# Kernel tuning notes

Measured on AMD Instinct MI355X. Metric: run time of the kernel, lower is better.

The kernel has to match this reference:

```python
import jax, jax.numpy as jnp
import numpy as np

N, DIN, D, K, H, N_ITERS = 16384, 256, 1024, 64, 2048, 3
THRESH = 0.3
EPS = 1e-8


def layernorm(x):
    mu = jnp.mean(x, axis=-1, keepdims=True)
    var = jnp.var(x, axis=-1, keepdims=True)
    return (x - mu) * jax.lax.rsqrt(var + 1e-5)


def setup_inputs() -> dict:
    key = jax.random.key(0)
    ks = jax.random.split(key, 20)
    s = 0.02
    return {
        "detections_t": jax.random.normal(ks[0], (N, DIN), jnp.float32),
        "detections_t1": jax.random.normal(ks[1], (N, DIN), jnp.float32),
        "W_enc": s * jax.random.normal(ks[2], (DIN, D), jnp.float32),
        "b_enc": jnp.zeros((D,), jnp.float32),
        "Wq": s * jax.random.normal(ks[3], (D, D), jnp.float32),
        "bq": jnp.zeros((D,), jnp.float32),
        "Wk": s * jax.random.normal(ks[4], (D, D), jnp.float32),
        "bk": jnp.zeros((D,), jnp.float32),
        "Wv": s * jax.random.normal(ks[5], (D, D), jnp.float32),
        "bv": jnp.zeros((D,), jnp.float32),
        "Wi": s * jax.random.normal(ks[6], (3 * D, D), jnp.float32),  # GRU input weights
        "Wh": s * jax.random.normal(ks[7], (3 * D, D), jnp.float32),  # GRU hidden weights
        "bi": jnp.zeros((3 * D,), jnp.float32),
        "bh": jnp.zeros((3 * D,), jnp.float32),
        "W1": s * jax.random.normal(ks[8], (D, H), jnp.float32),
        "b1": jnp.zeros((H,), jnp.float32),
        "W2": s * jax.random.normal(ks[9], (H, D), jnp.float32),
        "b2": jnp.zeros((D,), jnp.float32),
        "slots_mu": s * jax.random.normal(ks[10], (1, D), jnp.float32),
        "init_noise": jax.random.normal(ks[11], (K, D), jnp.float32) * s,
    }


def _gru(u, h, Wi, Wh, bi, bh):
    gi = u @ Wi.T + bi          # [K, 3D]
    gh = h @ Wh.T + bh
    ir, iz, inn = jnp.split(gi, 3, axis=-1)
    hr, hz, hn = jnp.split(gh, 3, axis=-1)
    r = jax.nn.sigmoid(ir + hr)
    z = jax.nn.sigmoid(iz + hz)
    n = jnp.tanh(inn + r * hn)
    return (1.0 - z) * n + z * h


def _process_frame(dets, prev_slots, p):
    x = layernorm(dets @ p["W_enc"] + p["b_enc"])          # [N, D]
    k = x @ p["Wk"] + p["bk"]                               # [N, D]
    v = x @ p["Wv"] + p["bv"]                               # [N, D]
    slots = prev_slots if prev_slots is not None else p["slots_mu"] + p["init_noise"]
    scale = D ** -0.5
    for _ in range(N_ITERS):
        slots_prev = slots
        q = layernorm(slots) @ p["Wq"] + p["bq"]            # [K, D]
        dots = (q @ k.T) * scale                             # [K, N]
        attn = jax.nn.softmax(dots, axis=0)                  # slots compete per detection
        attn = attn / (jnp.sum(attn, axis=-1, keepdims=True) + EPS)
        updates = attn @ v                                   # [K, D]
        slots = _gru(updates, slots_prev, p["Wi"], p["Wh"], p["bi"], p["bh"])
        slots = slots + (jax.nn.relu(layernorm(slots) @ p["W1"] + p["b1"]) @ p["W2"] + p["b2"])
    return slots


def _slot_similarity(a, b):
    an = a / (jnp.linalg.norm(a, axis=-1, keepdims=True) + EPS)
    bn = b / (jnp.linalg.norm(b, axis=-1, keepdims=True) + EPS)
    return an @ bn.T                                         # [K, K]


def _greedy_match(sim):
    max_sims = jnp.max(sim, axis=1)
    max_idxs = jnp.argmax(sim, axis=1)
    order = jnp.argsort(-max_sims)
    def step(carry, idx):
        matches, used = carry
        j = max_idxs[idx]
        ok = jnp.logical_and(~used[j], max_sims[idx] > THRESH)
        matches = matches.at[idx].set(jnp.where(ok, j, matches[idx]))
        used = used.at[j].set(used[j] | ok)
        return (matches, used), None
    init = (jnp.full((K,), -1, jnp.int32), jnp.zeros((K,), jnp.bool_))
    (matches, _), _ = jax.lax.scan(step, init, order)
    return matches


def reference(detections_t, detections_t1, W_enc, b_enc, Wq, bq, Wk, bk, Wv, bv,
              Wi, Wh, bi, bh, W1, b1, W2, b2, slots_mu, init_noise):
    p = dict(W_enc=W_enc, b_enc=b_enc, Wq=Wq, bq=bq, Wk=Wk, bk=bk, Wv=Wv, bv=bv,
             Wi=Wi, Wh=Wh, bi=bi, bh=bh, W1=W1, b1=b1, W2=W2, b2=b2,
             slots_mu=slots_mu, init_noise=init_noise)
    prev_slots = _process_frame(detections_t, None, p)
    curr_slots = _process_frame(detections_t1, prev_slots, p)
    sim = _slot_similarity(prev_slots, curr_slots)
    matches = _greedy_match(sim)
    return matches, sim
```

## Files before the change

kernel.cpp:

```cpp
#include <hip/hip_runtime.h>
#include <hip/hip_bf16.h>
#include <type_traits>

typedef __hip_bfloat16 bf16;
typedef __attribute__((ext_vector_type(8))) short s16x8;
typedef __attribute__((ext_vector_type(4))) float f32x4;

#define N_DET 16384
#define DIN   256
#define DD    1024
#define KSLOT 64
#define HH    2048
#define TD    3072

__device__ __forceinline__ float b2f(bf16 x){ return __bfloat162float(x); }
__device__ __forceinline__ bf16  f2b(float x){ return __float2bfloat16(x); }
__device__ __forceinline__ float bits2f(short u){ return __uint_as_float(((unsigned)(unsigned short)u) << 16); }

__device__ __forceinline__ void gload_lds16(const void* g, void* l) {
  __builtin_amdgcn_global_load_lds(
      (const __attribute__((address_space(1))) unsigned int*)g,
      (__attribute__((address_space(3))) unsigned int*)l, 16, 0, 0);
}

__device__ __forceinline__ void big_compute(bf16* As, bf16* Bs,
    const bf16* __restrict__ Ap, const bf16* __restrict__ Bp, int K, f32x4 acc[4][4])
{
  const int tid = threadIdx.x;
  const int lane = tid & 63, wave = tid >> 6;
  const int wr = wave >> 1, wc = wave & 1;
  const int l15 = lane & 15, h = lane >> 4;
  const int rr = tid >> 3;
  const int qs = ((tid & 7) ^ (rr & 7)) * 8;

#pragma unroll
  for (int m = 0; m < 4; ++m)
#pragma unroll
    for (int n = 0; n < 4; ++n) acc[m][n] = {0.f, 0.f, 0.f, 0.f};

  for (int k0 = 0; k0 < K; k0 += 64) {
    __syncthreads();
#pragma unroll
    for (int g = 0; g < 4; ++g)
      gload_lds16(Ap + (size_t)(g * 32 + rr) * K + k0 + qs,
                  As + ((size_t)g * 256 + wave * 64) * 8);
#pragma unroll
    for (int g = 0; g < 4; ++g)
      gload_lds16(Bp + (size_t)(g * 32 + rr) * K + k0 + qs,
                  Bs + ((size_t)g * 256 + wave * 64) * 8);
    __syncthreads();

#pragma unroll
    for (int ks = 0; ks < 2; ++ks) {
      s16x8 af[4], bfr[4];
#pragma unroll
      for (int m = 0; m < 4; ++m) {
        int row = wr * 64 + m * 16 + l15;
        af[m] = *(const s16x8*)&As[row * 64 + (((ks * 4 + h) ^ (l15 & 7)) * 8)];
      }
#pragma unroll
      for (int n = 0; n < 4; ++n) {
        int row = wc * 64 + n * 16 + l15;
        bfr[n] = *(const s16x8*)&Bs[row * 64 + (((ks * 4 + h) ^ (l15 & 7)) * 8)];
      }
#pragma unroll
      for (int m = 0; m < 4; ++m)
#pragma unroll
        for (int n = 0; n < 4; ++n)
          acc[m][n] = __builtin_amdgcn_mfma_f32_16x16x32_bf16(af[m], bfr[n], acc[m][n], 0, 0, 0);
    }
  }
}

__device__ __forceinline__ void big_gemm_body(int wg, int nct,
    const bf16* __restrict__ A, const bf16* __restrict__ Bt,
    const float* __restrict__ bias, bf16* __restrict__ C, int N, int K,
    bf16* As, bf16* Bs)
{
  const int bn = (wg % nct) * 128;
  const int bm = (wg / nct) * 128;
  f32x4 acc[4][4];
  big_compute(As, Bs, A + (size_t)bm * K, Bt + (size_t)bn * K, K, acc);

  const int lane = threadIdx.x & 63, wave = threadIdx.x >> 6;
  const int wr = wave >> 1, wc = wave & 1;
#pragma unroll
  for (int m = 0; m < 4; ++m)
#pragma unroll
    for (int n = 0; n < 4; ++n) {
      int col = bn + wc * 64 + n * 16 + (lane & 15);
      float bv = bias ? bias[col] : 0.f;
#pragma unroll
      for (int j = 0; j < 4; ++j) {
        int row = bm + wr * 64 + m * 16 + (lane >> 4) * 4 + j;
        C[(size_t)row * N + col] = f2b(acc[m][n][j] + bv);
      }
    }
}

__global__ __launch_bounds__(256) void gemm_mfma_bt(
    const bf16* __restrict__ A, const bf16* __restrict__ Bt,
    const float* __restrict__ bias, bf16* __restrict__ C, int M, int N, int K)
{
  const int nct = N >> 7;
  const int chunk = gridDim.x >> 3;
  const int wg = (blockIdx.x & 7) * chunk + (blockIdx.x >> 3);
  __shared__ bf16 As[128 * 64];
  __shared__ bf16 Bs[128 * 64];
  big_gemm_body(wg, nct, A, Bt, bias, C, N, K, As, Bs);
}

__global__ __launch_bounds__(256) void gemm_setup_pair(
    const bf16* __restrict__ Wi_b, const bf16* __restrict__ Wv_bf, bf16* __restrict__ Wvit,
    const bf16* __restrict__ Wk_bf, const bf16* __restrict__ Wq_bf, bf16* __restrict__ Wqk_t)
{
  __shared__ bf16 As[128 * 64];
  __shared__ bf16 Bs[128 * 64];
  if (blockIdx.x < 192) {
    int bid = blockIdx.x;
    int wg = (bid & 7) * 24 + (bid >> 3);
    big_gemm_body(wg, 8, Wi_b, Wv_bf, nullptr, Wvit, DD, DD, As, Bs);
  } else {
    int bid = blockIdx.x - 192;
    int wg = (bid & 7) * 8 + (bid >> 3);
    big_gemm_body(wg, 8, Wk_bf, Wq_bf, nullptr, Wqk_t, DD, DD, As, Bs);
  }
}

__device__ __forceinline__ void skinny_compute(bf16* As, bf16* Bs,
    const bf16* __restrict__ A, const bf16* __restrict__ Bt,
    int K, int Kc, int n0, int kb0, f32x4 acc[4])
{
  const int tid = threadIdx.x;
  const int lane = tid & 63, wave = tid >> 6;
  const int rem = wave * 64 + lane;
  const int r = rem >> 2, q = rem & 3;
  const int l15 = lane & 15, h = lane >> 4;

#pragma unroll
  for (int m = 0; m < 4; ++m) acc[m] = {0.f, 0.f, 0.f, 0.f};

  for (int kb = kb0; kb < kb0 + Kc; kb += 128) {
    __syncthreads();
#pragma unroll
    for (int g = 0; g < 4; ++g)
      gload_lds16(A + (size_t)r * K + kb + g * 32 + q * 8,
                  As + ((size_t)g * 256 + wave * 64) * 8);
#pragma unroll
    for (int g = 0; g < 4; ++g)
      gload_lds16(Bt + (size_t)(n0 + r) * K + kb + g * 32 + q * 8,
                  Bs + ((size_t)g * 256 + wave * 64) * 8);
    __syncthreads();

#pragma unroll
    for (int ks = 0; ks < 4; ++ks) {
      s16x8 bfr = *(const s16x8*)&Bs[(ks * 64 + wave * 16 + l15) * 32 + h * 8];
#pragma unroll
      for (int m = 0; m < 4; ++m) {
        s16x8 af = *(const s16x8*)&As[(ks * 64 + m * 16 + l15) * 32 + h * 8];
        acc[m] = __builtin_amdgcn_mfma_f32_16x16x32_bf16(af, bfr, acc[m], 0, 0, 0);
      }
    }
  }
}

template<int EPI>
__global__ __launch_bounds__(256) void gemm_skinny_e(
    const bf16* __restrict__ A, const bf16* __restrict__ Bt,
    float* __restrict__ pbuf, bf16* __restrict__ outb,
    const float* __restrict__ bias, int N, int K, int Kc)
{
  __shared__ bf16 As[4 * 64 * 32];
  __shared__ bf16 Bs[4 * 64 * 32];
  f32x4 acc[4];
  skinny_compute(As, Bs, A, Bt, K, Kc, blockIdx.x * 64, blockIdx.y * Kc, acc);

  const int lane = threadIdx.x & 63, wave = threadIdx.x >> 6;
  const int l15 = lane & 15, h = lane >> 4;
#pragma unroll
  for (int m = 0; m < 4; ++m)
#pragma unroll
    for (int j = 0; j < 4; ++j) {
      int row = m * 16 + h * 4 + j;
      int col = blockIdx.x * 64 + wave * 16 + l15;
      if (EPI == 0) {
        pbuf[((size_t)(blockIdx.y * 64) + row) * N + col] = acc[m][j];
      } else {
        float v = acc[m][j] + bias[col];
        if (EPI == 2) v = fmaxf(v, 0.f);
        outb[(size_t)row * N + col] = f2b(v);
      }
    }
}

__global__ __launch_bounds__(256) void gemm_skinny_dual(
    const bf16* __restrict__ A0, const bf16* __restrict__ A1,
    const bf16* __restrict__ B0, const bf16* __restrict__ B1,
    float* __restrict__ p0, float* __restrict__ p1, int N, int K, int Kc)
{
  __shared__ bf16 As[4 * 64 * 32];
  __shared__ bf16 Bs[4 * 64 * 32];
  const bf16* A = blockIdx.z ? A1 : A0;
  const bf16* B = blockIdx.z ? B1 : B0;
  float* p = blockIdx.z ? p1 : p0;

  f32x4 acc[4];
  skinny_compute(As, Bs, A, B, K, Kc, blockIdx.x * 64, blockIdx.y * Kc, acc);

  const int lane = threadIdx.x & 63, wave = threadIdx.x >> 6;
  const int l15 = lane & 15, h = lane >> 4;
#pragma unroll
  for (int m = 0; m < 4; ++m)
#pragma unroll
    for (int j = 0; j < 4; ++j) {
      int row = m * 16 + h * 4 + j;
      int col = blockIdx.x * 64 + wave * 16 + l15;
      p[((size_t)(blockIdx.y * 64) + row) * N + col] = acc[m][j];
    }
}

__device__ __forceinline__ void block_ln_store(float v[4], float s, float sq,
    bf16* __restrict__ out, int row,
    const float* __restrict__ wqbk, float* __restrict__ cbuf, float* __restrict__ colsum)
{
  for (int o = 32; o > 0; o >>= 1) { s += __shfl_down(s, o, 64); sq += __shfl_down(sq, o, 64); }
  __shared__ float ls[4], lq[4];
  int w = threadIdx.x >> 6;
  if ((threadIdx.x & 63) == 0) { ls[w] = s; lq[w] = sq; }
  __syncthreads();
  s  = ls[0] + ls[1] + ls[2] + ls[3];
  sq = lq[0] + lq[1] + lq[2] + lq[3];
  float mu = s * (1.f / DD);
  float var = sq * (1.f / DD) - mu * mu;
  float rstd = rsqrtf(var + 1e-5f);
#pragma unroll
  for (int j = 0; j < 4; j++)
    out[(size_t)row * DD + threadIdx.x + j * 256] = f2b((v[j] - mu) * rstd);
  if (wqbk) {
    float dot = 0.f;
#pragma unroll
    for (int j = 0; j < 4; j++) dot += (v[j] - mu) * rstd * wqbk[threadIdx.x + j * 256];
    for (int o = 32; o > 0; o >>= 1) dot += __shfl_down(dot, o, 64);
    __syncthreads();
    if ((threadIdx.x & 63) == 0) ls[w] = dot;
    __syncthreads();
    if (threadIdx.x == 0) { cbuf[row] = ls[0] + ls[1] + ls[2] + ls[3]; colsum[row] = 0.f; }
  }
}

__global__ __launch_bounds__(256) void gru_reduce_ln(const float* __restrict__ pA,
    const float* __restrict__ pB, const float* __restrict__ bvi,
    const float* __restrict__ bh, float* __restrict__ slots, bf16* __restrict__ lnb)
{
  int s = blockIdx.x, t = threadIdx.x;
  float v[4], sum = 0.f, sq = 0.f;
#pragma unroll
  for (int j = 0; j < 4; ++j) {
    int d = t + j * 256;
    const float* a = pA + (size_t)s * TD;
    const float* b = pB + (size_t)s * TD;
    float ir = bvi[d] + a[d], iz = bvi[1024 + d] + a[1024 + d], in_ = bvi[2048 + d] + a[2048 + d];
    float hr = bh[d] + b[d], hz = bh[1024 + d] + b[1024 + d], hnn = bh[2048 + d] + b[2048 + d];
    float r = 1.f / (1.f + expf(-(ir + hr)));
    float z = 1.f / (1.f + expf(-(iz + hz)));
    float nn = tanhf(in_ + r * hnn);
    float h = slots[(size_t)s * DD + d];
    float hv = (1.f - z) * nn + z * h;
    slots[(size_t)s * DD + d] = hv;
    v[j] = hv; sum += hv; sq += hv * hv;
  }
  block_ln_store(v, sum, sq, lnb, s, nullptr, nullptr, nullptr);
}

template<int SK>
__global__ __launch_bounds__(256) void mlp2_reduce_ln(const float* __restrict__ pbuf,
    const float* __restrict__ bias, float* __restrict__ slots,
    bf16* __restrict__ slotspb, bf16* __restrict__ lnb,
    const float* __restrict__ wqbk, float* __restrict__ cbuf, float* __restrict__ colsum)
{
  int s = blockIdx.x, t = threadIdx.x;
  float v[4], sum = 0.f, sq = 0.f;
#pragma unroll
  for (int j = 0; j < 4; ++j) {
    int d = t + j * 256;
    float x = bias[d] + slots[(size_t)s * DD + d];
#pragma unroll
    for (int sk = 0; sk < SK; ++sk) x += pbuf[(size_t)(sk * 64 + s) * DD + d];
    slots[(size_t)s * DD + d] = x;
    slotspb[(size_t)s * DD + d] = f2b(x);
    v[j] = x; sum += x; sq += x * x;
  }
  block_ln_store(v, sum, sq, lnb, s, wqbk, cbuf, colsum);
}

__global__ __launch_bounds__(256) void slots_init_ln(const float* __restrict__ mu,
    const float* __restrict__ noise, float* __restrict__ slots,
    bf16* __restrict__ slotspb, bf16* __restrict__ lnb,
    const float* __restrict__ wqbk, float* __restrict__ cbuf, float* __restrict__ colsum)
{
  int s = blockIdx.x, t = threadIdx.x;
  float v[4], sum = 0.f, sq = 0.f;
#pragma unroll
  for (int j = 0; j < 4; ++j) {
    int d = t + j * 256;
    float x = mu[d] + noise[(size_t)s * DD + d];
    slots[(size_t)s * DD + d] = x;
    slotspb[(size_t)s * DD + d] = f2b(x);
    v[j] = x; sum += x; sq += x * x;
  }
  block_ln_store(v, sum, sq, lnb, s, wqbk, cbuf, colsum);
}

__global__ __launch_bounds__(256) void qk_softmax(const bf16* __restrict__ qkb,
    const bf16* __restrict__ x, const float* __restrict__ cbuf,
    bf16* __restrict__ attn, float* __restrict__ colsum)
{
  __shared__ bf16 Qs[64 * 64];
  __shared__ bf16 Ks[64 * 64];
  __shared__ float cs[64], cl[64];
  const int t = threadIdx.x, lane = t & 63, wave = t >> 6;
  const int n0 = blockIdx.x * 64;
  const int l15 = lane & 15, h = lane >> 4;
  if (t < 64) { cs[t] = 0.f; cl[t] = cbuf[t]; }

  f32x4 acc[4];
#pragma unroll
  for (int m = 0; m < 4; ++m) acc[m] = {0.f, 0.f, 0.f, 0.f};

  for (int k0 = 0; k0 < DD; k0 += 64) {
    __syncthreads();
#pragma unroll
    for (int c = 0; c < 2; ++c) {
      int i = c * 256 + t;
      int r = i >> 3, q8 = i & 7;
      gload_lds16(qkb + (size_t)r * DD + k0 + q8 * 8, Qs + ((size_t)c * 256 + wave * 64) * 8);
    }
#pragma unroll
    for (int c = 0; c < 2; ++c) {
      int i = c * 256 + t;
      int r = i >> 3, q8 = i & 7;
      gload_lds16(x + (size_t)(n0 + r) * DD + k0 + q8 * 8, Ks + ((size_t)c * 256 + wave * 64) * 8);
    }
    __syncthreads();

#pragma unroll
    for (int ks = 0; ks < 2; ++ks) {
      s16x8 bfr = *(const s16x8*)&Ks[(wave * 16 + l15) * 64 + ks * 32 + h * 8];
#pragma unroll
      for (int m = 0; m < 4; ++m) {
        s16x8 af = *(const s16x8*)&Qs[(m * 16 + l15) * 64 + ks * 32 + h * 8];
        acc[m] = __builtin_amdgcn_mfma_f32_16x16x32_bf16(af, bfr, acc[m], 0, 0, 0);
      }
    }
  }

  float e[4][4];
  float cmax = -1e30f;
#pragma unroll
  for (int m = 0; m < 4; ++m)
#pragma unroll
    for (int j = 0; j < 4; ++j) {
      e[m][j] = (acc[m][j] + cl[m * 16 + h * 4 + j]) * 0.03125f;
      cmax = fmaxf(cmax, e[m][j]);
    }
  cmax = fmaxf(cmax, __shfl_xor(cmax, 16, 64));
  cmax = fmaxf(cmax, __shfl_xor(cmax, 32, 64));
  float ssum = 0.f;
#pragma unroll
  for (int m = 0; m < 4; ++m)
#pragma unroll
    for (int j = 0; j < 4; ++j) { e[m][j] = expf(e[m][j] - cmax); ssum += e[m][j]; }
  ssum += __shfl_xor(ssum, 16, 64);
  ssum += __shfl_xor(ssum, 32, 64);
  float inv = 1.f / ssum;
  __syncthreads();

  const int n = n0 + wave * 16 + l15;
#pragma unroll
  for (int m = 0; m < 4; ++m)
#pragma unroll
    for (int j = 0; j < 4; ++j) {
      float a = e[m][j] * inv;
      int s = m * 16 + h * 4 + j;
      attn[(size_t)s * N_DET + n] = f2b(a);
      float v = a;
      v += __shfl_xor(v, 1, 64);
      v += __shfl_xor(v, 2, 64);
      v += __shfl_xor(v, 4, 64);
      v += __shfl_xor(v, 8, 64);
      if (l15 == 0) atomicAdd(&cs[s], v);
    }
  __syncthreads();
  if (t < 64) atomicAdd(&colsum[t], cs[t]);
}

template<int SK>
__global__ __launch_bounds__(256) void updates_reduce2(const float* __restrict__ pbuf,
    const float* __restrict__ colsum, bf16* __restrict__ tb)
{
  int s = blockIdx.y, d = blockIdx.x * 256 + threadIdx.x;
  float v = 0.f;
#pragma unroll
  for (int sk = 0; sk < SK; ++sk) v += pbuf[(size_t)(sk * 64 + s) * DD + d];
  tb[(size_t)s * DD + d] = f2b(v / (colsum[s] + 1e-8f));
}

__global__ __launch_bounds__(256) void transpose_all(const float* __restrict__ W_enc,
    const float* __restrict__ W1, const float* __restrict__ W2,
    bf16* __restrict__ Wenc_t, bf16* __restrict__ W1_t, bf16* __restrict__ W2_t)
{
  __shared__ float t[32][33];
  int b = blockIdx.x;
  const float* W; bf16* Wt; int K, N, bx, by;
  if (b < 256)       { W = W_enc; Wt = Wenc_t; K = DIN;  N = DD; bx = b & 31;  by = b >> 5; }
  else if (b < 2304) { int r = b - 256;  W = W1; Wt = W1_t; K = DD;  N = HH; bx = r & 63; by = r >> 6; }
  else               { int r = b - 2304; W = W2; Wt = W2_t; K = HH;  N = DD; bx = r & 31; by = r >> 5; }
  int n0 = bx * 32, k0 = by * 32;
  int tx = threadIdx.x & 31, ty = threadIdx.x >> 5;
  for (int r = ty; r < 32; r += 8)
    t[r][tx] = W[(size_t)(k0 + r) * N + n0 + tx];
  __syncthreads();
  for (int r = ty; r < 32; r += 8)
    Wt[(size_t)(n0 + r) * K + k0 + tx] = f2b(t[tx][r]);
}

__global__ void f32_to_bf16_v(const float* __restrict__ in, bf16* __restrict__ out, int n)
{
  int i = (blockIdx.x * 256 + threadIdx.x) * 4;
  if (i < n) {
    float4 v = *(const float4*)(in + i);
    bf16 o[4] = {f2b(v.x), f2b(v.y), f2b(v.z), f2b(v.w)};
    *(ushort4*)(out + i) = *(const ushort4*)o;
  }
}

__global__ void convert_all(const float* __restrict__ Wh, const float* __restrict__ Wi,
    const float* __restrict__ Wv, const float* __restrict__ Wq, const float* __restrict__ Wk,
    bf16* __restrict__ oWh, bf16* __restrict__ oWi, bf16* __restrict__ oWv,
    bf16* __restrict__ oWq, bf16* __restrict__ oWk)
{
  int b = blockIdx.x;
  const float* src; bf16* dst; int base;
  if      (b < 3072) { src = Wh; dst = oWh; base = b; }
  else if (b < 6144) { src = Wi; dst = oWi; base = b - 3072; }
  else if (b < 7168) { src = Wv; dst = oWv; base = b - 6144; }
  else if (b < 8192) { src = Wq; dst = oWq; base = b - 7168; }
  else               { src = Wk; dst = oWk; base = b - 8192; }
  int i = (base * 256 + threadIdx.x) * 4;
  float4 v = *(const float4*)(src + i);
  bf16 o[4] = {f2b(v.x), f2b(v.y), f2b(v.z), f2b(v.w)};
  *(ushort4*)(dst + i) = *(const ushort4*)o;
}

__global__ __launch_bounds__(256) void matvec3_wave(const float* __restrict__ Wi,
    const float* __restrict__ Wq, const float* __restrict__ Wk,
    const float* __restrict__ bv, const float* __restrict__ bk, const float* __restrict__ bq,
    const float* __restrict__ bi,
    float* __restrict__ bvi, float* __restrict__ wqbk, float* __restrict__ bqk)
{
  int row = blockIdx.x * 4 + (threadIdx.x >> 6);
  int lane = threadIdx.x & 63;
  const float* w; const float* vec; float s0; float* out; int idx;
  if (row < 3072)      { idx = row;        w = Wi + (size_t)idx * DD; vec = bv; s0 = bi[idx]; out = bvi; }
  else if (row < 4096) { idx = row - 3072; w = Wq + (size_t)idx * DD; vec = bk; s0 = 0.f;     out = wqbk; }
  else                 { idx = row - 4096; w = Wk + (size_t)idx * DD; vec = bq; s0 = 0.f;     out = bqk; }
  float s = 0.f;
#pragma unroll
  for (int c = 0; c < 4; ++c) {
    float4 wv = *(const float4*)(w + c * 256 + lane * 4);
    float4 bb = *(const float4*)(vec + c * 256 + lane * 4);
    s += wv.x * bb.x + wv.y * bb.y + wv.z * bb.z + wv.w * bb.w;
  }
  for (int o = 32; o > 0; o >>= 1) s += __shfl_down(s, o, 64);
  if (lane == 0) out[idx] = s0 + s;
}

__global__ __launch_bounds__(256) void ln_transpose(const bf16* __restrict__ x_pre,
    bf16* __restrict__ x, bf16* __restrict__ xT)
{
  __shared__ bf16 tile[32][1032];
  __shared__ float mus[32], rs[32];
  const int t = threadIdx.x;
  const int n0 = blockIdx.x * 32;

#pragma unroll
  for (int i = 0; i < 16; ++i) {
    int flat = i * 256 + t;
    int row = flat >> 7, c8 = flat & 127;
    *(s16x8*)&tile[row][c8 * 8] = *(const s16x8*)&x_pre[(size_t)(n0 + row) * DD + c8 * 8];
  }
  __syncthreads();

  {
    int row = t >> 3, part = t & 7;
    float s = 0.f, sq = 0.f;
#pragma unroll
    for (int kk = 0; kk < 16; ++kk) {
      s16x8 v = *(const s16x8*)&tile[row][part * 128 + kk * 8];
#pragma unroll
      for (int j = 0; j < 8; ++j) { float f = bits2f(v[j]); s += f; sq += f * f; }
    }
    s  += __shfl_xor(s, 1, 64);  sq += __shfl_xor(sq, 1, 64);
    s  += __shfl_xor(s, 2, 64);  sq += __shfl_xor(sq, 2, 64);
    s  += __shfl_xor(s, 4, 64);  sq += __shfl_xor(sq, 4, 64);
    if (part == 0) {
      float mu = s * (1.f / DD);
      float var = sq * (1.f / DD) - mu * mu;
      mus[row] = mu;
      rs[row] = rsqrtf(var + 1e-5f);
    }
  }
  __syncthreads();

#pragma unroll
  for (int i = 0; i < 16; ++i) {
    int flat = i * 256 + t;
    int row = flat >> 7, c8 = flat & 127;
    float mu = mus[row], r = rs[row];
    s16x8 v = *(const s16x8*)&tile[row][c8 * 8];
    bf16 o[8];
#pragma unroll
    for (int j = 0; j < 8; ++j) o[j] = f2b((bits2f(v[j]) - mu) * r);
    *(s16x8*)&x[(size_t)(n0 + row) * DD + c8 * 8] = *(const s16x8*)o;
  }

#pragma unroll
  for (int i = 0; i < 16; ++i) {
    int flat = i * 256 + t;
    int d = flat >> 2, ch = flat & 3;
    bf16 o[8];
#pragma unroll
    for (int k = 0; k < 8; ++k) {
      int nl = ch * 8 + k;
      o[k] = f2b((b2f(tile[nl][d]) - mus[nl]) * rs[nl]);
    }
    *(s16x8*)&xT[(size_t)d * N_DET + n0 + ch * 8] = *(const s16x8*)o;
  }
}

__global__ __launch_bounds__(256) void rownorm2(const float* __restrict__ a,
    const float* __restrict__ b, float* __restrict__ an, float* __restrict__ bn)
{
  int rb = blockIdx.x;
  const float* p = (rb < 64 ? a : b) + (size_t)(rb & 63) * DD;
  float* o = (rb < 64 ? an : bn) + (size_t)(rb & 63) * DD;
  float v[4], sq = 0.f;
#pragma unroll
  for (int j = 0; j < 4; j++) { v[j] = p[threadIdx.x + j*256]; sq += v[j]*v[j]; }
  for (int os = 32; os > 0; os >>= 1) sq += __shfl_down(sq, os, 64);
  __shared__ float lq[4];
  int w = threadIdx.x >> 6;
  if ((threadIdx.x & 63) == 0) lq[w] = sq;
  __syncthreads();
  sq = lq[0] + lq[1] + lq[2] + lq[3];
  float sc = 1.f / (sqrtf(sq) + 1e-8f);
#pragma unroll
  for (int j = 0; j < 4; j++) o[threadIdx.x + j*256] = v[j] * sc;
}

__global__ __launch_bounds__(256) void sim_kernel(const float* __restrict__ an,
    const float* __restrict__ bn, float* __restrict__ simout)
{
  __shared__ float ar[1024];
  int i = blockIdx.x;
  for (int l = threadIdx.x; l < 1024; l += 256) ar[l] = an[(size_t)i * DD + l];
  __syncthreads();
  int j = threadIdx.x >> 2, g = threadIdx.x & 3;
  float sum = 0.f;
  for (int d = g; d < 1024; d += 4) sum += ar[d] * bn[(size_t)j * DD + d];
  sum += __shfl_xor(sum, 1, 64);
  sum += __shfl_xor(sum, 2, 64);
  if (g == 0) simout[i * 64 + j] = sum;
}

__global__ void match_kernel(const float* __restrict__ sim, float* __restrict__ outm)
{
  __shared__ float m[64];
  __shared__ int idx[64];
  __shared__ int order[64];
  __shared__ int used[64];
  int i = threadIdx.x;
  float best = -1e30f; int bj = 0;
  for (int j = 0; j < 64; j++) {
    float v = sim[i * 64 + j];
    if (v > best) { best = v; bj = j; }
  }
  m[i] = best; idx[i] = bj; used[i] = 0;
  __syncthreads();
  int cnt = 0;
  for (int j = 0; j < 64; j++) {
    float mj = m[j];
    if (mj > best || (mj == best && j < i)) cnt++;
  }
  order[cnt] = i;
  __syncthreads();
  if (i == 0) {
    for (int r = 0; r < 64; r++) {
      int ii = order[r];
      int j = idx[ii];
      bool ok = (!used[j]) && (m[ii] > 0.3f);
      outm[ii] = ok ? (float)j : -1.0f;
      if (ok) used[j] = 1;
    }
  }
}

static constexpr size_t OFF_XPRE = 0;
static constexpr size_t OFF_ATT  = 0;
static constexpr size_t OFF_PA   = (size_t)4  << 20;
static constexpr size_t OFF_P0   = (size_t)8  << 20;
static constexpr size_t OFF_P1   = (size_t)10 << 20;
static constexpr size_t OFF_WET  = (size_t)32 << 20;
static constexpr size_t OFF_WQKT = OFF_WET + ((size_t)512 << 10);
static constexpr size_t OFF_W1T  = OFF_WQKT + ((size_t)2 << 20);
static constexpr size_t OFF_W2T  = OFF_W1T + ((size_t)4 << 20);
static constexpr size_t OFF_WHB  = OFF_W2T + ((size_t)4 << 20);
static constexpr size_t OFF_WVIT = OFF_WHB + ((size_t)6 << 20);
static constexpr size_t OFF_X    = (size_t)60 << 20;
static constexpr size_t OFF_WIB  = OFF_X;
static constexpr size_t OFF_WVB  = OFF_X + ((size_t)6 << 20);
static constexpr size_t OFF_WQB  = OFF_X + ((size_t)8 << 20);
static constexpr size_t OFF_WKB  = OFF_X + ((size_t)10 << 20);
static constexpr size_t OFF_DBF  = OFF_X;
static constexpr size_t OFF_XT   = OFF_X + ((size_t)32 << 20);
static constexpr size_t OFF_SM   = OFF_XT + ((size_t)32 << 20);
static constexpr size_t OFF_SL   = OFF_SM;
static constexpr size_t OFF_SLPB = OFF_SL  + 262144;
static constexpr size_t OFF_LNB  = OFF_SLPB + 131072;
static constexpr size_t OFF_QKB  = OFF_LNB + 131072;
static constexpr size_t OFF_TB   = OFF_QKB + 131072;
static constexpr size_t OFF_HIDB = OFF_TB  + 131072;
static constexpr size_t OFF_PRV  = OFF_HIDB + 262144;
static constexpr size_t OFF_AN   = OFF_PRV + 262144;
static constexpr size_t OFF_BN   = OFF_AN  + 262144;
static constexpr size_t OFF_CS   = OFF_BN  + 262144;
static constexpr size_t OFF_BVI  = OFF_CS  + 4096;
static constexpr size_t OFF_WQBK = OFF_BVI + 16384;
static constexpr size_t OFF_BQK  = OFF_WQBK + 4096;

extern "C" void kernel_launch(void* const* d_in, const int* in_sizes, int n_in,
                              void* d_out, int out_size, void* d_ws, size_t ws_size,
                              hipStream_t stream)
{
  (void)in_sizes; (void)n_in; (void)out_size; (void)ws_size;
  const float* dets_t   = (const float*)d_in[0];
  const float* dets_t1  = (const float*)d_in[1];
  const float* W_enc    = (const float*)d_in[2];
  const float* b_enc    = (const float*)d_in[3];
  const float* Wq       = (const float*)d_in[4];
  const float* bq       = (const float*)d_in[5];
  const float* Wk       = (const float*)d_in[6];
  const float* bk       = (const float*)d_in[7];
  const float* Wv       = (const float*)d_in[8];
  const float* bv       = (const float*)d_in[9];
  const float* Wi       = (const float*)d_in[10];
  const float* Wh       = (const float*)d_in[11];
  const float* bi       = (const float*)d_in[12];
  const float* bh       = (const float*)d_in[13];
  const float* W1       = (const float*)d_in[14];
  const float* b1       = (const float*)d_in[15];
  const float* W2       = (const float*)d_in[16];
  const float* b2       = (const float*)d_in[17];
  const float* slots_mu = (const float*)d_in[18];
  const float* init_noise = (const float*)d_in[19];

  char* ws = (char*)d_ws;
  bf16*  x_pre  = (bf16*)(ws + OFF_XPRE);
  bf16*  attn   = (bf16*)(ws + OFF_ATT);
  float* pA     = (float*)(ws + OFF_PA);
  float* p0     = (float*)(ws + OFF_P0);
  float* p1     = (float*)(ws + OFF_P1);
  bf16*  Wenc_t = (bf16*)(ws + OFF_WET);
  bf16*  Wqk_t  = (bf16*)(ws + OFF_WQKT);
  bf16*  W1_t   = (bf16*)(ws + OFF_W1T);
  bf16*  W2_t   = (bf16*)(ws + OFF_W2T);
  bf16*  Wh_b   = (bf16*)(ws + OFF_WHB);
  bf16*  Wvit   = (bf16*)(ws + OFF_WVIT);
  bf16*  Wi_b   = (bf16*)(ws + OFF_WIB);
  bf16*  Wv_bf  = (bf16*)(ws + OFF_WVB);
  bf16*  Wq_bf  = (bf16*)(ws + OFF_WQB);
  bf16*  Wk_bf  = (bf16*)(ws + OFF_WKB);
  bf16*  dets_bf= (bf16*)(ws + OFF_DBF);
  bf16*  x      = (bf16*)(ws + OFF_X);
  bf16*  xT     = (bf16*)(ws + OFF_XT);
  float* slots  = (float*)(ws + OFF_SL);
  bf16*  slotspb= (bf16*)(ws + OFF_SLPB);
  bf16*  lnb    = (bf16*)(ws + OFF_LNB);
  bf16*  qkb    = (bf16*)(ws + OFF_QKB);
  bf16*  tb     = (bf16*)(ws + OFF_TB);
  bf16*  hidb   = (bf16*)(ws + OFF_HIDB);
  float* prevs  = (float*)(ws + OFF_PRV);
  float* an     = (float*)(ws + OFF_AN);
  float* bn     = (float*)(ws + OFF_BN);
  float* colsum = (float*)(ws + OFF_CS);
  float* cbuf   = colsum + 64;
  float* bvi    = (float*)(ws + OFF_BVI);
  float* wqbk   = (float*)(ws + OFF_WQBK);
  float* bqk    = (float*)(ws + OFF_BQK);

  transpose_all<<<4352, 256, 0, stream>>>(W_enc, W1, W2, Wenc_t, W1_t, W2_t);
  convert_all<<<9216, 256, 0, stream>>>(Wh, Wi, Wv, Wq, Wk, Wh_b, Wi_b, Wv_bf, Wq_bf, Wk_bf);
  matvec3_wave<<<1280, 256, 0, stream>>>(Wi, Wq, Wk, bv, bk, bq, bi, bvi, wqbk, bqk);
  gemm_setup_pair<<<256, 256, 0, stream>>>(Wi_b, Wv_bf, Wvit, Wk_bf, Wq_bf, Wqk_t);

  auto frame = [&](const float* dets, bool first) {
    f32_to_bf16_v<<<(N_DET*DIN)/1024, 256, 0, stream>>>(dets, dets_bf, N_DET*DIN);
    gemm_mfma_bt<<<1024, 256, 0, stream>>>(dets_bf, Wenc_t, b_enc, x_pre, N_DET, DD, DIN);
    ln_transpose<<<512, 256, 0, stream>>>(x_pre, x, xT);
    if (first) slots_init_ln<<<64, 256, 0, stream>>>(slots_mu, init_noise, slots, slotspb, lnb, wqbk, cbuf, colsum);
    for (int it = 0; it < 3; ++it) {
      gemm_skinny_e<1><<<dim3(16, 1), 256, 0, stream>>>(lnb, Wqk_t, nullptr, qkb, bqk, DD, DD, DD);
      qk_softmax<<<256, 256, 0, stream>>>(qkb, x, cbuf, attn, colsum);
      gemm_skinny_e<0><<<dim3(16, 16), 256, 0, stream>>>(attn, xT, pA, nullptr, nullptr, DD, N_DET, 1024);
      updates_reduce2<16><<<dim3(4, 64), 256, 0, stream>>>(pA, colsum, tb);
      gemm_skinny_dual<<<dim3(48, 1, 2), 256, 0, stream>>>(tb, slotspb, Wvit, Wh_b, p0, p1, TD, DD, DD);
      gru_reduce_ln<<<64, 256, 0, stream>>>(p0, p1, bvi, bh, slots, lnb);
      gemm_skinny_e<2><<<dim3(32, 1), 256, 0, stream>>>(lnb, W1_t, nullptr, hidb, b1, HH, DD, DD);
      gemm_skinny_e<0><<<dim3(16, 2), 256, 0, stream>>>(hidb, W2_t, pA, nullptr, nullptr, DD, HH, 1024);
      mlp2_reduce_ln<2><<<64, 256, 0, stream>>>(pA, b2, slots, slotspb, lnb, wqbk, cbuf, colsum);
    }
  };

  frame(dets_t, true);
  hipMemcpyAsync(prevs, slots, 262144, hipMemcpyDeviceToDevice, stream);
  frame(dets_t1, false);

  rownorm2<<<128, 256, 0, stream>>>(prevs, slots, an, bn);
  float* outf = (float*)d_out;
  sim_kernel<<<KSLOT, 256, 0, stream>>>(an, bn, outf + 64);
  match_kernel<<<1, 64, 0, stream>>>(outf + 64, outf);
}
```

Before: 667.0 us.

## Split LayerNorm transpose into stats pass and tiled normalize-transpose; drop memcpy

The single ln_transpose kernel (32-row blocks holding a full 1024-wide row in LDS, with strided column reads for the transpose) is replaced by two kernels. A per-row stats kernel computes mean and rstd with one wave per row. A 64x64 tiled kernel then normalizes, writes x, and writes xT through a small padded LDS tile, which gives far more blocks and smaller LDS use. The device-to-device memcpy of the first frame's slots is also removed; the last mlp2_reduce_ln of frame one writes prevs directly. The cost is reading x_pre twice and one extra launch.

```diff
diff --git a/kernel.cpp b/kernel.cpp
--- a/kernel.cpp
+++ b/kernel.cpp
@@ -276,7 +276,8 @@
 __global__ __launch_bounds__(256) void mlp2_reduce_ln(const float* __restrict__ pbuf,
     const float* __restrict__ bias, float* __restrict__ slots,
     bf16* __restrict__ slotspb, bf16* __restrict__ lnb,
-    const float* __restrict__ wqbk, float* __restrict__ cbuf, float* __restrict__ colsum)
+    const float* __restrict__ wqbk, float* __restrict__ cbuf, float* __restrict__ colsum,
+    float* __restrict__ prevs)
 {
   int s = blockIdx.x, t = threadIdx.x;
   float v[4], sum = 0.f, sq = 0.f;
@@ -288,6 +289,7 @@
     for (int sk = 0; sk < SK; ++sk) x += pbuf[(size_t)(sk * 64 + s) * DD + d];
     slots[(size_t)s * DD + d] = x;
     slotspb[(size_t)s * DD + d] = f2b(x);
+    if (prevs) prevs[(size_t)s * DD + d] = x;
     v[j] = x; sum += x; sq += x * x;
   }
   block_ln_store(v, sum, sq, lnb, s, wqbk, cbuf, colsum);
@@ -475,67 +477,53 @@
   if (lane == 0) out[idx] = s0 + s;
 }
 
-__global__ __launch_bounds__(256) void ln_transpose(const bf16* __restrict__ x_pre,
-    bf16* __restrict__ x, bf16* __restrict__ xT)
-{
-  __shared__ bf16 tile[32][1032];
-  __shared__ float mus[32], rs[32];
-  const int t = threadIdx.x;
-  const int n0 = blockIdx.x * 32;
-
-#pragma unroll
-  for (int i = 0; i < 16; ++i) {
-    int flat = i * 256 + t;
-    int row = flat >> 7, c8 = flat & 127;
-    *(s16x8*)&tile[row][c8 * 8] = *(const s16x8*)&x_pre[(size_t)(n0 + row) * DD + c8 * 8];
-  }
-  __syncthreads();
-
-  {
-    int row = t >> 3, part = t & 7;
-    float s = 0.f, sq = 0.f;
-#pragma unroll
-    for (int kk = 0; kk < 16; ++kk) {
-      s16x8 v = *(const s16x8*)&tile[row][part * 128 + kk * 8];
-#pragma unroll
-      for (int j = 0; j < 8; ++j) { float f = bits2f(v[j]); s += f; sq += f * f; }
-    }
-    s  += __shfl_xor(s, 1, 64);  sq += __shfl_xor(sq, 1, 64);
-    s  += __shfl_xor(s, 2, 64);  sq += __shfl_xor(sq, 2, 64);
-    s  += __shfl_xor(s, 4, 64);  sq += __shfl_xor(sq, 4, 64);
-    if (part == 0) {
-      float mu = s * (1.f / DD);
-      float var = sq * (1.f / DD) - mu * mu;
-      mus[row] = mu;
-      rs[row] = rsqrtf(var + 1e-5f);
-    }
-  }
-  __syncthreads();
-
-#pragma unroll
-  for (int i = 0; i < 16; ++i) {
-    int flat = i * 256 + t;
-    int row = flat >> 7, c8 = flat & 127;
-    float mu = mus[row], r = rs[row];
-    s16x8 v = *(const s16x8*)&tile[row][c8 * 8];
-    bf16 o[8];
-#pragma unroll
-    for (int j = 0; j < 8; ++j) o[j] = f2b((bits2f(v[j]) - mu) * r);
-    *(s16x8*)&x[(size_t)(n0 + row) * DD + c8 * 8] = *(const s16x8*)o;
-  }
-
-#pragma unroll
-  for (int i = 0; i < 16; ++i) {
-    int flat = i * 256 + t;
-    int d = flat >> 2, ch = flat & 3;
-    bf16 o[8];
-#pragma unroll
-    for (int k = 0; k < 8; ++k) {
-      int nl = ch * 8 + k;
-      o[k] = f2b((b2f(tile[nl][d]) - mus[nl]) * rs[nl]);
-    }
-    *(s16x8*)&xT[(size_t)d * N_DET + n0 + ch * 8] = *(const s16x8*)o;
-  }
+__global__ __launch_bounds__(256) void ln_stats(const bf16* __restrict__ x_pre,
+                                                float2* __restrict__ stats)
+{
+  int row = blockIdx.x * 4 + (threadIdx.x >> 6);
+  int lane = threadIdx.x & 63;
+  const bf16* p = x_pre + (size_t)row * DD + lane * 16;
+  s16x8 v0 = *(const s16x8*)p;
+  s16x8 v1 = *(const s16x8*)(p + 8);
+  float s = 0.f, sq = 0.f;
+#pragma unroll
+  for (int j = 0; j < 8; ++j) {
+    float a = bits2f(v0[j]), b = bits2f(v1[j]);
+    s += a + b; sq += a * a + b * b;
+  }
+  for (int o = 32; o > 0; o >>= 1) { s += __shfl_down(s, o, 64); sq += __shfl_down(sq, o, 64); }
+  if (lane == 0) {
+    float mu = s * (1.f / DD);
+    float var = sq * (1.f / DD) - mu * mu;
+    stats[row] = make_float2(mu, rsqrtf(var + 1e-5f));
+  }
+}
+
+__global__ __launch_bounds__(256) void norm_transpose(const bf16* __restrict__ x_pre,
+    const float2* __restrict__ stats, bf16* __restrict__ x, bf16* __restrict__ xT)
+{
+  __shared__ bf16 t[64][70];
+  int n0 = blockIdx.x * 64, d0 = blockIdx.y * 64;
+  int r = threadIdx.x >> 2, c = (threadIdx.x & 3) * 16;
+  float2 st = stats[n0 + r];
+  s16x8 v0 = *(const s16x8*)&x_pre[(size_t)(n0 + r) * DD + d0 + c];
+  s16x8 v1 = *(const s16x8*)&x_pre[(size_t)(n0 + r) * DD + d0 + c + 8];
+  bf16 o16[16];
+#pragma unroll
+  for (int j = 0; j < 8; ++j) {
+    o16[j]     = f2b((bits2f(v0[j]) - st.x) * st.y);
+    o16[8 + j] = f2b((bits2f(v1[j]) - st.x) * st.y);
+  }
+  *(s16x8*)&x[(size_t)(n0 + r) * DD + d0 + c]     = *(const s16x8*)&o16[0];
+  *(s16x8*)&x[(size_t)(n0 + r) * DD + d0 + c + 8] = *(const s16x8*)&o16[8];
+#pragma unroll
+  for (int j = 0; j < 16; ++j) t[c + j][r] = o16[j];
+  __syncthreads();
+  bf16 o[16];
+#pragma unroll
+  for (int j = 0; j < 16; ++j) o[j] = t[r][c + j];
+  *(s16x8*)&xT[(size_t)(d0 + r) * N_DET + n0 + c]     = *(const s16x8*)&o[0];
+  *(s16x8*)&xT[(size_t)(d0 + r) * N_DET + n0 + c + 8] = *(const s16x8*)&o[8];
 }
 
 __global__ __launch_bounds__(256) void rownorm2(const float* __restrict__ a,
@@ -637,6 +625,7 @@
 static constexpr size_t OFF_BVI  = OFF_CS  + 4096;
 static constexpr size_t OFF_WQBK = OFF_BVI + 16384;
 static constexpr size_t OFF_BQK  = OFF_WQBK + 4096;
+static constexpr size_t OFF_STAT = OFF_BQK + 4096;
 
 extern "C" void kernel_launch(void* const* d_in, const int* in_sizes, int n_in,
                               void* d_out, int out_size, void* d_ws, size_t ws_size,
@@ -697,6 +686,7 @@
   float* bvi    = (float*)(ws + OFF_BVI);
   float* wqbk   = (float*)(ws + OFF_WQBK);
   float* bqk    = (float*)(ws + OFF_BQK);
+  float2* stats = (float2*)(ws + OFF_STAT);
 
   transpose_all<<<4352, 256, 0, stream>>>(W_enc, W1, W2, Wenc_t, W1_t, W2_t);
   convert_all<<<9216, 256, 0, stream>>>(Wh, Wi, Wv, Wq, Wk, Wh_b, Wi_b, Wv_bf, Wq_bf, Wk_bf);
@@ -706,7 +696,8 @@
   auto frame = [&](const float* dets, bool first) {
     f32_to_bf16_v<<<(N_DET*DIN)/1024, 256, 0, stream>>>(dets, dets_bf, N_DET*DIN);
     gemm_mfma_bt<<<1024, 256, 0, stream>>>(dets_bf, Wenc_t, b_enc, x_pre, N_DET, DD, DIN);
-    ln_transpose<<<512, 256, 0, stream>>>(x_pre, x, xT);
+    ln_stats<<<4096, 256, 0, stream>>>(x_pre, stats);
+    norm_transpose<<<dim3(256, 16), 256, 0, stream>>>(x_pre, stats, x, xT);
     if (first) slots_init_ln<<<64, 256, 0, stream>>>(slots_mu, init_noise, slots, slotspb, lnb, wqbk, cbuf, colsum);
     for (int it = 0; it < 3; ++it) {
       gemm_skinny_e<1><<<dim3(16, 1), 256, 0, stream>>>(lnb, Wqk_t, nullptr, qkb, bqk, DD, DD, DD);
@@ -717,12 +708,12 @@
       gru_reduce_ln<<<64, 256, 0, stream>>>(p0, p1, bvi, bh, slots, lnb);
       gemm_skinny_e<2><<<dim3(32, 1), 256, 0, stream>>>(lnb, W1_t, nullptr, hidb, b1, HH, DD, DD);
       gemm_skinny_e<0><<<dim3(16, 2), 256, 0, stream>>>(hidb, W2_t, pA, nullptr, nullptr, DD, HH, 1024);
-      mlp2_reduce_ln<2><<<64, 256, 0, stream>>>(pA, b2, slots, slotspb, lnb, wqbk, cbuf, colsum);
+      mlp2_reduce_ln<2><<<64, 256, 0, stream>>>(pA, b2, slots, slotspb, lnb, wqbk, cbuf, colsum,
+                                                (first && it == 2) ? prevs : nullptr);
     }
   };
 
   frame(dets_t, true);
-  hipMemcpyAsync(prevs, slots, 262144, hipMemcpyDeviceToDevice, stream);
   frame(dets_t1, false);
 
   rownorm2<<<128, 256, 0, stream>>>(prevs, slots, an, bn);
```

After: 685.2 us. 1.03x slower.
